# Optimization experiments

Hardware: AMD Instinct MI355X
Metric: run time of the kernel (lower is better)

## Reference

```python
import jax, jax.numpy as jnp
import numpy as np

D_MODEL = 768
D_STATE = 16
D_CONV = 4
EXPAND = 2
D_INNER = EXPAND * D_MODEL  # 1536
DT_RANK = (D_MODEL + 15) // 16  # 48, mamba_ssm default dt_rank='auto'
BATCH = 2
SEQ = 2048


def setup_inputs() -> dict:
    key = jax.random.key(0)
    ks = jax.random.split(key, 9)
    f = lambda k, shp, s=0.02: (jax.random.normal(k, shp, jnp.float32) * s)
    return {
        "x": jax.random.normal(ks[0], (BATCH, SEQ, D_MODEL), jnp.float32),
        "ln_w": jnp.ones((D_MODEL,), jnp.float32),
        "ln_b": jnp.zeros((D_MODEL,), jnp.float32),
        "in_proj_w": f(ks[1], (2 * D_INNER, D_MODEL)),          # no bias (mamba default)
        "conv_w": f(ks[2], (D_INNER, D_CONV), 0.1),              # depthwise causal conv
        "conv_b": f(ks[3], (D_INNER,), 0.1),
        "x_proj_w": f(ks[4], (DT_RANK + 2 * D_STATE, D_INNER)),  # no bias
        "dt_proj_w": f(ks[5], (D_INNER, DT_RANK), 0.1),
        "dt_proj_b": f(ks[6], (D_INNER,), 0.5),
        "A_log": jnp.log(jnp.broadcast_to(
            jnp.arange(1, D_STATE + 1, dtype=jnp.float32), (D_INNER, D_STATE))),  # S4D-real init
        "D": jnp.ones((D_INNER,), jnp.float32),
        "out_proj_w": f(ks[7], (D_MODEL, D_INNER)),              # no bias
    }


def _layernorm(x, w, b, eps=1e-5):
    mu = jnp.mean(x, axis=-1, keepdims=True)
    var = jnp.var(x, axis=-1, keepdims=True)
    return (x - mu) * jax.lax.rsqrt(var + eps) * w + b


def _mamba(xn, in_proj_w, conv_w, conv_b, x_proj_w, dt_proj_w, dt_proj_b,
           A_log, D, out_proj_w):
    B, L, _ = xn.shape
    # input projection -> gate z and ssm branch u
    xz = jnp.einsum("bld,ed->ble", xn, in_proj_w)  # [B,L,2*d_inner]
    u, z = jnp.split(xz, 2, axis=-1)
    # causal depthwise conv1d (kernel D_CONV, left pad D_CONV-1) + SiLU
    up = jnp.pad(u, ((0, 0), (D_CONV - 1, 0), (0, 0)))
    uc = conv_b
    for k in range(D_CONV):  # small fixed tap loop
        uc = uc + conv_w[:, k] * up[:, k:k + L, :]
    uc = jax.nn.silu(uc)  # [B,L,d_inner]
    # data-dependent dt, B, C
    dbl = jnp.einsum("bld,ed->ble", uc, x_proj_w)
    dt, Bm, Cm = jnp.split(dbl, [DT_RANK, DT_RANK + D_STATE], axis=-1)
    delta = jax.nn.softplus(jnp.einsum("blr,dr->bld", dt, dt_proj_w) + dt_proj_b)
    A = -jnp.exp(A_log)  # [d_inner, d_state]

    def step(h, inp):
        u_t, d_t, B_t, C_t = inp  # [B,d_inner],[B,d_inner],[B,d_state],[B,d_state]
        dA = jnp.exp(d_t[..., None] * A)                      # [B,d_inner,d_state]
        h = dA * h + (d_t * u_t)[..., None] * B_t[:, None, :]  # discretized update
        y = jnp.einsum("bds,bs->bd", h, C_t)
        return h, y

    h0 = jnp.zeros((B, D_INNER, D_STATE), xn.dtype)
    xs = (uc.transpose(1, 0, 2), delta.transpose(1, 0, 2),
          Bm.transpose(1, 0, 2), Cm.transpose(1, 0, 2))
    _, ys = jax.lax.scan(step, h0, xs)          # ys: [L,B,d_inner]
    y = ys.transpose(1, 0, 2) + uc * D          # skip connection D*u
    y = y * jax.nn.silu(z)                      # gating
    return jnp.einsum("bld,od->blo", y, out_proj_w)


def reference(x, ln_w, ln_b, in_proj_w, conv_w, conv_b, x_proj_w,
              dt_proj_w, dt_proj_b, A_log, D, out_proj_w):
    xn = _layernorm(x, ln_w, ln_b)
    return x + _mamba(xn, in_proj_w, conv_w, conv_b, x_proj_w,
                      dt_proj_w, dt_proj_b, A_log, D, out_proj_w)
```

## Files before the change

### kernel.cpp

```cpp
#include <hip/hip_runtime.h>
#include <hip/hip_bf16.h>
#include <stdint.h>
#include <math.h>

typedef __hip_bfloat16 bf16;
typedef __attribute__((ext_vector_type(8))) short bf16x8;
typedef __attribute__((ext_vector_type(4))) short s16x4;
typedef __attribute__((ext_vector_type(4))) float f32x4;

#define B_   2
#define L_   2048
#define DM   768
#define DI   1536
#define DS   16
#define M_   (B_ * L_)
#define NC   128
#define LC   (L_ / NC)
#define NSEQ (B_ * DI * DS)
#define KSPLIT 12
#define LOG2E  1.44269504088896f
#define NLOG2E (-1.44269504088896f)

#define GLOAD_LDS16(g, l)                                                     \
  __builtin_amdgcn_global_load_lds(                                           \
      (const __attribute__((address_space(1))) void*)(g),                     \
      (__attribute__((address_space(3))) void*)(l), 16, 0, 0)

__device__ inline float bf2f(short s) {
  union { unsigned int u; float f; } c;
  c.u = ((unsigned int)(unsigned short)s) << 16;
  return c.f;
}

__global__ __launch_bounds__(256) void k_prep(
    const float* __restrict__ x, const float* __restrict__ w,
    const float* __restrict__ b, bf16* __restrict__ xnb,
    const float* __restrict__ ipw, const float* __restrict__ xpw,
    const float* __restrict__ dpw, const float* __restrict__ opw,
    bf16* __restrict__ wib, bf16* __restrict__ wxb,
    bf16* __restrict__ wdb, bf16* __restrict__ wob) {
  const int tid = threadIdx.x;
  if (blockIdx.x < M_) {
    const int m = blockIdx.x;
    const float* row = x + (size_t)m * DM;
    float v0 = row[tid], v1 = row[tid + 256], v2 = row[tid + 512];
    float s1 = v0 + v1 + v2;
    float s2 = v0 * v0 + v1 * v1 + v2 * v2;
    for (int mm = 1; mm < 64; mm <<= 1) {
      s1 += __shfl_xor(s1, mm);
      s2 += __shfl_xor(s2, mm);
    }
    __shared__ float r1s[4], r2s[4];
    int wv = tid >> 6, ln = tid & 63;
    if (ln == 0) { r1s[wv] = s1; r2s[wv] = s2; }
    __syncthreads();
    s1 = r1s[0] + r1s[1] + r1s[2] + r1s[3];
    s2 = r2s[0] + r2s[1] + r2s[2] + r2s[3];
    float mu = s1 * (1.f / 768.f);
    float var = s2 * (1.f / 768.f) - mu * mu;
    float rs = rsqrtf(var + 1e-5f);
    bf16* orow = xnb + (size_t)m * DM;
    orow[tid]       = __float2bfloat16((v0 - mu) * rs * w[tid]       + b[tid]);
    orow[tid + 256] = __float2bfloat16((v1 - mu) * rs * w[tid + 256] + b[tid + 256]);
    orow[tid + 512] = __float2bfloat16((v2 - mu) * rs * w[tid + 512] + b[tid + 512]);
    return;
  }
  const int n1 = 3072 * 768;
  const int n2 = 768 * 1536;
  const int n3 = 128 * 1536;
  const int n4 = 1536 * 64;
  const int total4 = (n1 + n2 + n3 + n4) / 4;
  const int stride = 512 * 256;
  for (int i4 = (blockIdx.x - M_) * 256 + tid; i4 < total4; i4 += stride) {
    int i = i4 * 4;
    f32x4 v = {0.f, 0.f, 0.f, 0.f};
    bf16* dst;
    if (i < n1) {
      v = *(const f32x4*)&ipw[i];
      dst = &wib[i];
    } else if (i < n1 + n2) {
      int j = i - n1;
      v = *(const f32x4*)&opw[j];
      dst = &wob[j];
    } else if (i < n1 + n2 + n3) {
      int j = i - n1 - n2;
      int r = j / 1536, c = j - r * 1536;
      if (r < 80) v = *(const f32x4*)&xpw[r * 1536 + c];
      dst = &wxb[j];
    } else {
      int j = i - n1 - n2 - n3;
      int r = j >> 6, c = j & 63;
      if (c < 48) v = *(const f32x4*)&dpw[r * 48 + c];
      dst = &wdb[j];
    }
    bf16 t[4];
#pragma unroll
    for (int k = 0; k < 4; ++k) t[k] = __float2bfloat16(v[k]);
    *(s16x4*)dst = *(const s16x4*)t;
  }
}

__device__ __forceinline__ void g256_stage_half(
    const bf16* __restrict__ g, int base_row, int K, int k0,
    short* lhalf, int wid, int lane) {
#pragma unroll
  for (int q = 0; q < 2; ++q) {
    int row_l = q * 64 + wid * 8 + (lane >> 3);
    int slot = (lane & 7) ^ (lane >> 3);
    GLOAD_LDS16(g + (size_t)(base_row + row_l) * K + k0 + slot * 8,
                lhalf + q * 4096 + wid * 512);
  }
}

__device__ __forceinline__ bf16x8 g256_ld(const short* bufop, int h, int row_l,
                                          int kk, int lane) {
  int kslot = (kk >> 3) + (lane >> 4);
  int off = h * 8192 + row_l * 64 + ((kslot ^ (lane & 7)) << 3);
  return *(const bf16x8*)&bufop[off];
}

__global__ __launch_bounds__(512) void k_gemm256(
    const bf16* __restrict__ A, const bf16* __restrict__ Bw, int K,
    bf16* __restrict__ C, int ldc) {
  __shared__ short lds[4 * 16384];
  short* A0 = lds;
  short* A1 = lds + 16384;
  short* B0 = lds + 32768;
  short* B1 = lds + 49152;
  const int tid = threadIdx.x, lane = tid & 63, wid = tid >> 6;
  const int wm_i = wid >> 2, wn_i = wid & 3;
  const int m0 = blockIdx.y * 256, n0 = blockIdx.x * 256;
  const int NT = K >> 6;

  f32x4 acc[8][4] = {};

  g256_stage_half(A, m0, K, 0, A0, wid, lane);
  g256_stage_half(A, m0 + 128, K, 0, A0 + 8192, wid, lane);
  g256_stage_half(Bw, n0, K, 0, B0, wid, lane);
  g256_stage_half(Bw, n0 + 128, K, 0, B0 + 8192, wid, lane);
  g256_stage_half(Bw, n0, K, 64, B1, wid, lane);
  g256_stage_half(Bw, n0 + 128, K, 64, B1 + 8192, wid, lane);
  asm volatile("s_waitcnt vmcnt(4)" ::: "memory");
  __builtin_amdgcn_s_barrier();

  for (int t = 0; t < NT; ++t) {
    short* Ab = (t & 1) ? A1 : A0;
    short* Bb = (t & 1) ? B1 : B0;
    short* Anx = (t & 1) ? A0 : A1;

    bf16x8 bfrag[4][2], afr[2][2];
#pragma unroll
    for (int nf = 0; nf < 4; ++nf) {
      int row_l = (wn_i & 1) * 64 + nf * 16 + (lane & 15);
      bfrag[nf][0] = g256_ld(Bb, wn_i >> 1, row_l, 0, lane);
      bfrag[nf][1] = g256_ld(Bb, wn_i >> 1, row_l, 32, lane);
    }
#pragma unroll
    for (int mf = 0; mf < 2; ++mf) {
      int row_l = mf * 16 + (lane & 15);
      afr[mf][0] = g256_ld(Ab, wm_i, row_l, 0, lane);
      afr[mf][1] = g256_ld(Ab, wm_i, row_l, 32, lane);
    }
    if (t + 1 < NT) {
      g256_stage_half(A, m0, K, (t + 1) * 64, Anx, wid, lane);
      g256_stage_half(A, m0 + 128, K, (t + 1) * 64, Anx + 8192, wid, lane);
    }
    __builtin_amdgcn_s_barrier();
    asm volatile("s_waitcnt lgkmcnt(0)" ::: "memory");
    __builtin_amdgcn_sched_barrier(0);
    __builtin_amdgcn_s_setprio(1);
#pragma unroll
    for (int mf = 0; mf < 2; ++mf)
#pragma unroll
      for (int nf = 0; nf < 4; ++nf) {
        acc[mf][nf] = __builtin_amdgcn_mfma_f32_16x16x32_bf16(
            afr[mf][0], bfrag[nf][0], acc[mf][nf], 0, 0, 0);
        acc[mf][nf] = __builtin_amdgcn_mfma_f32_16x16x32_bf16(
            afr[mf][1], bfrag[nf][1], acc[mf][nf], 0, 0, 0);
      }
    __builtin_amdgcn_s_setprio(0);
    __builtin_amdgcn_s_barrier();

#pragma unroll
    for (int p = 1; p < 4; ++p) {
      bf16x8 af2[2][2];
#pragma unroll
      for (int i = 0; i < 2; ++i) {
        int row_l = (p * 2 + i) * 16 + (lane & 15);
        af2[i][0] = g256_ld(Ab, wm_i, row_l, 0, lane);
        af2[i][1] = g256_ld(Ab, wm_i, row_l, 32, lane);
      }
      if (p < 3) {
        if (t + 2 < NT)
          g256_stage_half(Bw, n0 + (p - 1) * 128, K, (t + 2) * 64,
                          Bb + (p - 1) * 8192, wid, lane);
      } else {
        if (t + 2 < NT) {
          asm volatile("s_waitcnt vmcnt(4)" ::: "memory");
        } else {
          asm volatile("s_waitcnt vmcnt(0)" ::: "memory");
        }
      }
      __builtin_amdgcn_s_barrier();
      asm volatile("s_waitcnt lgkmcnt(0)" ::: "memory");
      __builtin_amdgcn_sched_barrier(0);
      __builtin_amdgcn_s_setprio(1);
#pragma unroll
      for (int i = 0; i < 2; ++i) {
        int mf = p * 2 + i;
#pragma unroll
        for (int nf = 0; nf < 4; ++nf) {
          acc[mf][nf] = __builtin_amdgcn_mfma_f32_16x16x32_bf16(
              af2[i][0], bfrag[nf][0], acc[mf][nf], 0, 0, 0);
          acc[mf][nf] = __builtin_amdgcn_mfma_f32_16x16x32_bf16(
              af2[i][1], bfrag[nf][1], acc[mf][nf], 0, 0, 0);
        }
      }
      __builtin_amdgcn_s_setprio(0);
      __builtin_amdgcn_s_barrier();
    }
  }

#pragma unroll
  for (int mf = 0; mf < 8; ++mf) {
    int row = m0 + wm_i * 128 + mf * 16 + ((lane >> 4) << 2);
#pragma unroll
    for (int nf = 0; nf < 4; ++nf) {
      int col = n0 + wn_i * 64 + nf * 16 + (lane & 15);
#pragma unroll
      for (int r = 0; r < 4; ++r)
        C[(size_t)(row + r) * ldc + col] = __float2bfloat16(acc[mf][nf][r]);
    }
  }
}

template <int EPI>
__global__ __launch_bounds__(256) void k_gemm_bt(
    const bf16* __restrict__ A, const bf16* __restrict__ Bw, int M, int N, int K,
    void* __restrict__ Cv, int ldc, const float* __restrict__ aux) {
  __shared__ short As[128 * 64];
  __shared__ short Bs[128 * 64];
  const int tid = threadIdx.x, lane = tid & 63, wv = tid >> 6;

  int bidx = blockIdx.x, bidy = blockIdx.y;
  if (gridDim.z == 1 && (gridDim.y & 7) == 0) {
    const int nx = gridDim.x;
    const int phys = bidy * nx + bidx;
    const int xcd = phys & 7, slot = phys >> 3;
    const int mt_per = gridDim.y >> 3;
    bidy = xcd * mt_per + slot / nx;
    bidx = slot % nx;
  }
  const int m0 = bidy * 128, n0 = bidx * 128;

  const int wm = (wv >> 1) * 64, wn = (wv & 1) * 64;
  const int lrow = lane >> 3, lcol8 = (lane & 7) * 8;
  const int ksl = K / gridDim.z;
  const int koff = ksl * blockIdx.z;

  f32x4 acc[4][4] = {};

  for (int k0 = koff; k0 < koff + ksl; k0 += 64) {
    __syncthreads();
#pragma unroll
    for (int j = 0; j < 4; ++j) {
      int reg = j * 4 + wv;
      int r = reg * 8 + lrow;
      GLOAD_LDS16(A + (size_t)(m0 + r) * K + k0 + lcol8, &As[reg * 8 * 64]);
      GLOAD_LDS16(Bw + (size_t)(n0 + r) * K + k0 + lcol8, &Bs[reg * 8 * 64]);
    }
    asm volatile("s_waitcnt vmcnt(0)" ::: "memory");
    __syncthreads();
#pragma unroll
    for (int kk = 0; kk < 64; kk += 32) {
      bf16x8 af[4], bfr[4];
#pragma unroll
      for (int i = 0; i < 4; ++i)
        af[i] = *(const bf16x8*)&As[(wm + i * 16 + (lane & 15)) * 64 + kk + ((lane >> 4) * 8)];
#pragma unroll
      for (int j = 0; j < 4; ++j)
        bfr[j] = *(const bf16x8*)&Bs[(wn + j * 16 + (lane & 15)) * 64 + kk + ((lane >> 4) * 8)];
#pragma unroll
      for (int i = 0; i < 4; ++i)
#pragma unroll
        for (int j = 0; j < 4; ++j)
          acc[i][j] = __builtin_amdgcn_mfma_f32_16x16x32_bf16(af[i], bfr[j], acc[i][j], 0, 0, 0);
    }
  }

  const size_t zoff = (size_t)blockIdx.z * M * ldc;
#pragma unroll
  for (int i = 0; i < 4; ++i) {
    int row_b = m0 + wm + i * 16 + ((lane >> 4) << 2);
#pragma unroll
    for (int j = 0; j < 4; ++j) {
      int col = n0 + wn + j * 16 + (lane & 15);
#pragma unroll
      for (int r = 0; r < 4; ++r) {
        int row = row_b + r;
        float v = acc[i][j][r];
        if (EPI == 0) {
          ((float*)Cv)[zoff + (size_t)row * ldc + col] = v;
        } else if (EPI == 1) {
          ((bf16*)Cv)[(size_t)row * ldc + col] = __float2bfloat16(v);
        } else if (EPI == 2) {
          float t = v + aux[col];
          float sp = fmaxf(t, 0.f) + __logf(1.f + __expf(-fabsf(t)));
          ((bf16*)Cv)[(size_t)row * ldc + col] = __float2bfloat16(sp);
        } else if (EPI == 3) {
          ((float*)Cv)[(size_t)row * ldc + col] = v + aux[(size_t)row * ldc + col];
        } else {
          ((bf16*)Cv)[zoff + (size_t)row * ldc + col] = __float2bfloat16(v);
        }
      }
    }
  }
}

__global__ __launch_bounds__(256) void k_conv(const bf16* __restrict__ xzb,
                                              const float* __restrict__ cw,
                                              const float* __restrict__ cb,
                                              bf16* __restrict__ ucb) {
  const int idx = blockIdx.x * 256 + threadIdx.x;
  const int mp = idx / (DI / 8);
  const int d8 = (idx - mp * (DI / 8)) * 8;
  const int m0 = mp * 2;
  const int tl = m0 & (L_ - 1);

  float wgt[8][4];
#pragma unroll
  for (int j = 0; j < 8; ++j) {
    f32x4 w4 = *(const f32x4*)&cw[(d8 + j) * 4];
#pragma unroll
    for (int k = 0; k < 4; ++k) wgt[j][k] = w4[k];
  }
  const f32x4* cbv = (const f32x4*)&cb[d8];
  f32x4 cb0 = cbv[0], cb1 = cbv[1];
  float acc0[8], acc1[8];
#pragma unroll
  for (int j = 0; j < 4; ++j) {
    acc0[j] = cb0[j]; acc0[4 + j] = cb1[j];
    acc1[j] = cb0[j]; acc1[4 + j] = cb1[j];
  }

  bf16x8 v[5];
  const bf16x8 z8 = (bf16x8)(short)0;
#pragma unroll
  for (int k = 0; k < 5; ++k) {
    int tt = tl - 3 + k;
    v[k] = (tt >= 0) ? *(const bf16x8*)&xzb[(size_t)(m0 - 3 + k) * 3072 + d8] : z8;
  }
#pragma unroll
  for (int k = 0; k < 4; ++k)
#pragma unroll
    for (int j = 0; j < 8; ++j) {
      acc0[j] += wgt[j][k] * bf2f(v[k][j]);
      acc1[j] += wgt[j][k] * bf2f(v[k + 1][j]);
    }

  bf16 o0[8], o1[8];
#pragma unroll
  for (int j = 0; j < 8; ++j) {
    o0[j] = __float2bfloat16(acc0[j] / (1.f + __expf(-acc0[j])));
    o1[j] = __float2bfloat16(acc1[j] / (1.f + __expf(-acc1[j])));
  }
  *(bf16x8*)&ucb[(size_t)m0 * DI + d8]       = *(bf16x8*)o0;
  *(bf16x8*)&ucb[(size_t)(m0 + 1) * DI + d8] = *(bf16x8*)o1;
}

__global__ __launch_bounds__(256) void k_xred(const float* __restrict__ xpart,
                                              float* __restrict__ dbl,
                                              bf16* __restrict__ dtb) {
  const int idx = blockIdx.x * 256 + threadIdx.x;
  const int m = idx >> 7, c = idx & 127;
  float sum = 0.f;
#pragma unroll
  for (int s = 0; s < KSPLIT; ++s) sum += xpart[(size_t)s * (M_ * 128) + idx];
  dbl[idx] = sum;
  if (c < 64) dtb[m * 64 + c] = __float2bfloat16(c < 48 ? sum : 0.f);
}

__global__ __launch_bounds__(256) void k_ored(const bf16* __restrict__ op,
                                              const float* __restrict__ x,
                                              float* __restrict__ out) {
  const int i8 = (blockIdx.x * 256 + threadIdx.x) * 8;
  bf16x8 p0 = *(const bf16x8*)&op[i8];
  bf16x8 p1 = *(const bf16x8*)&op[(size_t)M_ * DM + i8];
  const f32x4* xp = (const f32x4*)&x[i8];
  f32x4 x0 = xp[0], x1 = xp[1];
  f32x4 o0, o1;
#pragma unroll
  for (int j = 0; j < 4; ++j) {
    o0[j] = x0[j] + bf2f(p0[j])     + bf2f(p1[j]);
    o1[j] = x1[j] + bf2f(p0[4 + j]) + bf2f(p1[4 + j]);
  }
  f32x4* outp = (f32x4*)&out[i8];
  outp[0] = o0;
  outp[1] = o1;
}

#define DA_CHAIN(dtval)                                                       \
  float r1 = __builtin_amdgcn_exp2f((dtval) * NLOG2E);                        \
  float r2 = r1 * r1, r3 = r2 * r1, r4 = r2 * r2;                             \
  float r5 = r4 * r1, r6 = r4 * r2, r7 = r4 * r3, r8 = r4 * r4;               \
  float dA[16] = {r1, r2, r3, r4, r5, r6, r7, r8,                             \
                  r8 * r1, r8 * r2, r8 * r3, r8 * r4,                         \
                  r8 * r5, r8 * r6, r8 * r7, r8 * r8};

__global__ __launch_bounds__(256) void k_scan1(
    const bf16* __restrict__ dlt, const bf16* __restrict__ ucb,
    const float* __restrict__ dbl,
    bf16* __restrict__ Qb, float* __restrict__ dts) {
  const int blk = blockIdx.x;
  const int cg = blk % (DI / 256);
  const int ch = (blk / (DI / 256)) % NC;
  const int b  = blk / ((DI / 256) * NC);
  const int d  = cg * 256 + threadIdx.x;
  const int t0 = ch * LC;
  __shared__ float sB[LC][16];
  {
    int t = threadIdx.x >> 4, j = threadIdx.x & 15;
    sB[t][j] = dbl[(size_t)(b * L_ + t0 + t) * 128 + 48 + j];
  }
  const bf16* dp = dlt + (size_t)(b * L_ + t0) * DI + d;
  const bf16* up = ucb + (size_t)(b * L_ + t0) * DI + d;
  float dtv[LC], uv[LC];
#pragma unroll
  for (int t = 0; t < LC; ++t) {
    dtv[t] = __bfloat162float(dp[(size_t)t * DI]);
    uv[t]  = __bfloat162float(up[(size_t)t * DI]);
  }
  float h[16];
#pragma unroll
  for (int s = 0; s < 16; ++s) h[s] = 0.f;
  __syncthreads();
  float dtsum = 0.f;
#pragma unroll
  for (int t = 0; t < LC; ++t) {
    float du = dtv[t] * uv[t];
    dtsum += dtv[t];
    const f32x4* bp = (const f32x4*)&sB[t][0];
    f32x4 Bv[4] = {bp[0], bp[1], bp[2], bp[3]};
    DA_CHAIN(dtv[t]);
#pragma unroll
    for (int s = 0; s < 16; ++s)
      h[s] = dA[s] * h[s] + du * Bv[s >> 2][s & 3];
  }
  size_t base = (size_t)ch * NSEQ + (size_t)(b * DI + d) * DS;
  bf16 qs[16];
#pragma unroll
  for (int s = 0; s < 16; ++s) qs[s] = __float2bfloat16(h[s]);
  *(bf16x8*)&Qb[base]     = *(bf16x8*)&qs[0];
  *(bf16x8*)&Qb[base + 8] = *(bf16x8*)&qs[8];
  dts[(size_t)ch * (B_ * DI) + b * DI + d] = dtsum;
}

__global__ __launch_bounds__(256) void k_scan2(const bf16* __restrict__ Qb,
                                               bf16* __restrict__ Hb,
                                               const float* __restrict__ dts,
                                               const float* __restrict__ A_log) {
  const int gid = blockIdx.x * 256 + threadIdx.x;
  const int bd0 = (blockIdx.x * 256) >> 4;
  __shared__ float sDts[NC][16];
  for (int i = threadIdx.x; i < NC * 16; i += 256) {
    int c = i >> 4, k = i & 15;
    sDts[c][k] = dts[(size_t)c * (B_ * DI) + bd0 + k];
  }
  const float a2 = -__expf(A_log[gid % (DI * DS)]) * LOG2E;
  const int bdl = threadIdx.x >> 4;
  __syncthreads();
  float h = 0.f;
  for (int c0 = 0; c0 < NC; c0 += 8) {
    float q[8];
#pragma unroll
    for (int k = 0; k < 8; ++k)
      q[k] = __bfloat162float(Qb[(size_t)(c0 + k) * NSEQ + gid]);
#pragma unroll
    for (int k = 0; k < 8; ++k) {
      float P = __builtin_amdgcn_exp2f(a2 * sDts[c0 + k][bdl]);
      Hb[(size_t)(c0 + k) * NSEQ + gid] = __float2bfloat16(h);
      h = P * h + q[k];
    }
  }
}

__global__ __launch_bounds__(256) void k_scan3(
    const bf16* __restrict__ dlt, const bf16* __restrict__ ucb,
    const bf16* __restrict__ xzb, const float* __restrict__ dbl,
    const float* __restrict__ Dp,
    const bf16* __restrict__ Hb, bf16* __restrict__ ybf) {
  const int blk = blockIdx.x;
  const int cg = blk % (DI / 256);
  const int ch = (blk / (DI / 256)) % NC;
  const int b  = blk / ((DI / 256) * NC);
  const int d  = cg * 256 + threadIdx.x;
  const int t0 = ch * LC;
  __shared__ float sBC[LC][32];
  for (int i = threadIdx.x; i < LC * 32; i += 256) {
    int t = i >> 5, j = i & 31;
    sBC[t][j] = dbl[(size_t)(b * L_ + t0 + t) * 128 + 48 + j];
  }
  const bf16* dp = dlt + (size_t)(b * L_ + t0) * DI + d;
  const bf16* up = ucb + (size_t)(b * L_ + t0) * DI + d;
  const bf16* zp = xzb + (size_t)(b * L_ + t0) * 3072 + DI + d;
  float dtv[LC], uv[LC], zv[LC];
#pragma unroll
  for (int t = 0; t < LC; ++t) {
    dtv[t] = __bfloat162float(dp[(size_t)t * DI]);
    uv[t]  = __bfloat162float(up[(size_t)t * DI]);
    zv[t]  = __bfloat162float(zp[(size_t)t * 3072]);
  }
  float h[16];
  const bf16* Hp = Hb + (size_t)ch * NSEQ + (size_t)(b * DI + d) * DS;
  bf16x8 h0 = *(const bf16x8*)&Hp[0];
  bf16x8 h1 = *(const bf16x8*)&Hp[8];
#pragma unroll
  for (int s = 0; s < 16; ++s) h[s] = bf2f(s < 8 ? h0[s] : h1[s - 8]);
  const float Dd = Dp[d];
  __syncthreads();
  bf16* yp = ybf + (size_t)(b * L_ + t0) * DI + d;
#pragma unroll
  for (int t = 0; t < LC; ++t) {
    float du = dtv[t] * uv[t];
    const f32x4* bc = (const f32x4*)&sBC[t][0];
    f32x4 Bv[4]  = {bc[0], bc[1], bc[2], bc[3]};
    f32x4 Cv4[4] = {bc[4], bc[5], bc[6], bc[7]};
    DA_CHAIN(dtv[t]);
    float y = 0.f;
#pragma unroll
    for (int s = 0; s < 16; ++s) {
      h[s] = dA[s] * h[s] + du * Bv[s >> 2][s & 3];
      y += h[s] * Cv4[s >> 2][s & 3];
    }
    y += Dd * uv[t];
    float g = zv[t] / (1.f + __expf(-zv[t]));
    yp[(size_t)t * DI] = __float2bfloat16(y * g);
  }
}

extern "C" void kernel_launch(void* const* d_in, const int* in_sizes, int n_in,
                              void* d_out, int out_size, void* d_ws, size_t ws_size,
                              hipStream_t stream) {
  const float* x    = (const float*)d_in[0];
  const float* lnw  = (const float*)d_in[1];
  const float* lnb  = (const float*)d_in[2];
  const float* ipw  = (const float*)d_in[3];
  const float* cw   = (const float*)d_in[4];
  const float* cb   = (const float*)d_in[5];
  const float* xpw  = (const float*)d_in[6];
  const float* dpw  = (const float*)d_in[7];
  const float* dpb  = (const float*)d_in[8];
  const float* alog = (const float*)d_in[9];
  const float* Dp   = (const float*)d_in[10];
  const float* opw  = (const float*)d_in[11];

  char* p = (char*)d_ws;
  auto alloc = [&](size_t bytes) {
    char* r = p;
    p += (bytes + 255) & ~(size_t)255;
    return r;
  };
  bf16* xnb  = (bf16*)alloc((size_t)M_ * DM * 2);
  bf16* wib  = (bf16*)alloc((size_t)3072 * 768 * 2);
  bf16* wxb  = (bf16*)alloc((size_t)128 * 1536 * 2);
  bf16* wdb  = (bf16*)alloc((size_t)1536 * 64 * 2);
  bf16* wob  = (bf16*)alloc((size_t)768 * 1536 * 2);
  bf16* xzb  = (bf16*)alloc((size_t)M_ * 3072 * 2);
  bf16* ucb  = (bf16*)alloc((size_t)M_ * DI * 2);
  float* dbl = (float*)alloc((size_t)M_ * 128 * 4);
  bf16* dtb  = (bf16*)alloc((size_t)M_ * 64 * 2);
  bf16* dlt  = (bf16*)alloc((size_t)M_ * DI * 2);
  bf16* ybf  = (bf16*)alloc((size_t)M_ * DI * 2);
  bf16* Qb   = (bf16*)alloc((size_t)NC * NSEQ * 2);
  bf16* Hb   = (bf16*)alloc((size_t)NC * NSEQ * 2);
  float* dts = (float*)alloc((size_t)NC * B_ * DI * 4);
  float* xpart = (float*)Qb;
  bf16* opart = Qb;

  k_prep<<<M_ + 512, 256, 0, stream>>>(x, lnw, lnb, xnb, ipw, xpw, dpw, opw,
                                       wib, wxb, wdb, wob);

  dim3 g1(3072 / 256, M_ / 256);
  k_gemm256<<<g1, 512, 0, stream>>>(xnb, wib, 768, xzb, 3072);

  k_conv<<<(M_ / 2) * (DI / 8) / 256, 256, 0, stream>>>(xzb, cw, cb, ucb);

  dim3 g2(1, M_ / 128, KSPLIT);
  k_gemm_bt<0><<<g2, 256, 0, stream>>>(ucb, wxb, M_, 128, 1536, xpart, 128, nullptr);

  k_xred<<<(M_ * 128) / 256, 256, 0, stream>>>(xpart, dbl, dtb);

  dim3 g3(1536 / 128, M_ / 128);
  k_gemm_bt<2><<<g3, 256, 0, stream>>>(dtb, wdb, M_, 1536, 64, dlt, 1536, dpb);

  const int nblk = B_ * NC * (DI / 256);
  k_scan1<<<nblk, 256, 0, stream>>>(dlt, ucb, dbl, Qb, dts);
  k_scan2<<<NSEQ / 256, 256, 0, stream>>>(Qb, Hb, dts, alog);
  k_scan3<<<nblk, 256, 0, stream>>>(dlt, ucb, xzb, dbl, Dp, Hb, ybf);

  dim3 g4(768 / 128, M_ / 128, 2);
  k_gemm_bt<4><<<g4, 256, 0, stream>>>(ybf, wob, M_, 768, 1536, opart, 768, nullptr);

  k_ored<<<(M_ * DM / 8) / 256, 256, 0, stream>>>(opart, x, (float*)d_out);
}
```

Baseline: 152.0 us.

## Restructure 256 GEMM main loop, swizzle block order, store x_proj partials in bf16

The 256x256 in_proj GEMM main loop drops from four sub-phases with barriers to two larger phases per K-tile, each doing 32 MFMAs. B-tile prefetches move into the two phases. A blockIdx remap spreads consecutive workgroups across XCD-sized groups to improve L2 locality. The split-K x_proj GEMM now writes bf16 partials (EPI 4) instead of fp32, which halves partial traffic at the cost of precision in the reduced dt/B/C values. The larger fragment arrays raise register pressure.

```diff
diff --git a/kernel.cpp b/kernel.cpp
--- a/kernel.cpp
+++ b/kernel.cpp
@@ -123,32 +123,44 @@
     const bf16* __restrict__ A, const bf16* __restrict__ Bw, int K,
     bf16* __restrict__ C, int ldc) {
   __shared__ short lds[4 * 16384];
-  short* A0 = lds;
-  short* A1 = lds + 16384;
-  short* B0 = lds + 32768;
-  short* B1 = lds + 49152;
+  short* Abuf0 = lds;
+  short* Abuf1 = lds + 16384;
+  short* Bbuf0 = lds + 32768;
+  short* Bbuf1 = lds + 49152;
   const int tid = threadIdx.x, lane = tid & 63, wid = tid >> 6;
   const int wm_i = wid >> 2, wn_i = wid & 3;
-  const int m0 = blockIdx.y * 256, n0 = blockIdx.x * 256;
+
+  int bidx = blockIdx.x, bidy = blockIdx.y;
+  {
+    int nx = gridDim.x;
+    int nwg = nx * gridDim.y;
+    if ((nwg & 7) == 0) {
+      int phys = bidy * nx + bidx;
+      int lin = (phys & 7) * (nwg >> 3) + (phys >> 3);
+      bidy = lin / nx;
+      bidx = lin - bidy * nx;
+    }
+  }
+  const int m0 = bidy * 256, n0 = bidx * 256;
   const int NT = K >> 6;
 
   f32x4 acc[8][4] = {};
 
-  g256_stage_half(A, m0, K, 0, A0, wid, lane);
-  g256_stage_half(A, m0 + 128, K, 0, A0 + 8192, wid, lane);
-  g256_stage_half(Bw, n0, K, 0, B0, wid, lane);
-  g256_stage_half(Bw, n0 + 128, K, 0, B0 + 8192, wid, lane);
-  g256_stage_half(Bw, n0, K, 64, B1, wid, lane);
-  g256_stage_half(Bw, n0 + 128, K, 64, B1 + 8192, wid, lane);
+  g256_stage_half(A, m0, K, 0, Abuf0, wid, lane);
+  g256_stage_half(A, m0 + 128, K, 0, Abuf0 + 8192, wid, lane);
+  g256_stage_half(Bw, n0, K, 0, Bbuf0, wid, lane);
+  g256_stage_half(Bw, n0 + 128, K, 0, Bbuf0 + 8192, wid, lane);
+  g256_stage_half(Bw, n0, K, 64, Bbuf1, wid, lane);
+  g256_stage_half(Bw, n0 + 128, K, 64, Bbuf1 + 8192, wid, lane);
   asm volatile("s_waitcnt vmcnt(4)" ::: "memory");
   __builtin_amdgcn_s_barrier();
 
   for (int t = 0; t < NT; ++t) {
-    short* Ab = (t & 1) ? A1 : A0;
-    short* Bb = (t & 1) ? B1 : B0;
-    short* Anx = (t & 1) ? A0 : A1;
-
-    bf16x8 bfrag[4][2], afr[2][2];
+    short* Ab  = (t & 1) ? Abuf1 : Abuf0;
+    short* Bb  = (t & 1) ? Bbuf1 : Bbuf0;
+    short* Anx = (t & 1) ? Abuf0 : Abuf1;
+
+    bf16x8 bfrag[4][2], afA[4][2];
 #pragma unroll
     for (int nf = 0; nf < 4; ++nf) {
       int row_l = (wn_i & 1) * 64 + nf * 16 + (lane & 15);
@@ -156,69 +168,57 @@
       bfrag[nf][1] = g256_ld(Bb, wn_i >> 1, row_l, 32, lane);
     }
 #pragma unroll
-    for (int mf = 0; mf < 2; ++mf) {
+    for (int mf = 0; mf < 4; ++mf) {
       int row_l = mf * 16 + (lane & 15);
-      afr[mf][0] = g256_ld(Ab, wm_i, row_l, 0, lane);
-      afr[mf][1] = g256_ld(Ab, wm_i, row_l, 32, lane);
+      afA[mf][0] = g256_ld(Ab, wm_i, row_l, 0, lane);
+      afA[mf][1] = g256_ld(Ab, wm_i, row_l, 32, lane);
     }
     if (t + 1 < NT) {
       g256_stage_half(A, m0, K, (t + 1) * 64, Anx, wid, lane);
       g256_stage_half(A, m0 + 128, K, (t + 1) * 64, Anx + 8192, wid, lane);
     }
+    asm volatile("s_waitcnt lgkmcnt(0)" ::: "memory");
     __builtin_amdgcn_s_barrier();
-    asm volatile("s_waitcnt lgkmcnt(0)" ::: "memory");
-    __builtin_amdgcn_sched_barrier(0);
+    if (t + 2 < NT)
+      g256_stage_half(Bw, n0, K, (t + 2) * 64, Bb, wid, lane);
     __builtin_amdgcn_s_setprio(1);
 #pragma unroll
-    for (int mf = 0; mf < 2; ++mf)
+    for (int mf = 0; mf < 4; ++mf)
 #pragma unroll
       for (int nf = 0; nf < 4; ++nf) {
         acc[mf][nf] = __builtin_amdgcn_mfma_f32_16x16x32_bf16(
-            afr[mf][0], bfrag[nf][0], acc[mf][nf], 0, 0, 0);
+            afA[mf][0], bfrag[nf][0], acc[mf][nf], 0, 0, 0);
         acc[mf][nf] = __builtin_amdgcn_mfma_f32_16x16x32_bf16(
-            afr[mf][1], bfrag[nf][1], acc[mf][nf], 0, 0, 0);
+            afA[mf][1], bfrag[nf][1], acc[mf][nf], 0, 0, 0);
       }
     __builtin_amdgcn_s_setprio(0);
+
+    bf16x8 afB[4][2];
+#pragma unroll
+    for (int mf = 0; mf < 4; ++mf) {
+      int row_l = (mf + 4) * 16 + (lane & 15);
+      afB[mf][0] = g256_ld(Ab, wm_i, row_l, 0, lane);
+      afB[mf][1] = g256_ld(Ab, wm_i, row_l, 32, lane);
+    }
+    if (t + 2 < NT)
+      g256_stage_half(Bw, n0 + 128, K, (t + 2) * 64, Bb + 8192, wid, lane);
+    __builtin_amdgcn_s_setprio(1);
+#pragma unroll
+    for (int mf = 0; mf < 4; ++mf)
+#pragma unroll
+      for (int nf = 0; nf < 4; ++nf) {
+        acc[mf + 4][nf] = __builtin_amdgcn_mfma_f32_16x16x32_bf16(
+            afB[mf][0], bfrag[nf][0], acc[mf + 4][nf], 0, 0, 0);
+        acc[mf + 4][nf] = __builtin_amdgcn_mfma_f32_16x16x32_bf16(
+            afB[mf][1], bfrag[nf][1], acc[mf + 4][nf], 0, 0, 0);
+      }
+    __builtin_amdgcn_s_setprio(0);
+    if (t + 2 < NT) {
+      asm volatile("s_waitcnt vmcnt(4)" ::: "memory");
+    } else {
+      asm volatile("s_waitcnt vmcnt(0)" ::: "memory");
+    }
     __builtin_amdgcn_s_barrier();
-
-#pragma unroll
-    for (int p = 1; p < 4; ++p) {
-      bf16x8 af2[2][2];
-#pragma unroll
-      for (int i = 0; i < 2; ++i) {
-        int row_l = (p * 2 + i) * 16 + (lane & 15);
-        af2[i][0] = g256_ld(Ab, wm_i, row_l, 0, lane);
-        af2[i][1] = g256_ld(Ab, wm_i, row_l, 32, lane);
-      }
-      if (p < 3) {
-        if (t + 2 < NT)
-          g256_stage_half(Bw, n0 + (p - 1) * 128, K, (t + 2) * 64,
-                          Bb + (p - 1) * 8192, wid, lane);
-      } else {
-        if (t + 2 < NT) {
-          asm volatile("s_waitcnt vmcnt(4)" ::: "memory");
-        } else {
-          asm volatile("s_waitcnt vmcnt(0)" ::: "memory");
-        }
-      }
-      __builtin_amdgcn_s_barrier();
-      asm volatile("s_waitcnt lgkmcnt(0)" ::: "memory");
-      __builtin_amdgcn_sched_barrier(0);
-      __builtin_amdgcn_s_setprio(1);
-#pragma unroll
-      for (int i = 0; i < 2; ++i) {
-        int mf = p * 2 + i;
-#pragma unroll
-        for (int nf = 0; nf < 4; ++nf) {
-          acc[mf][nf] = __builtin_amdgcn_mfma_f32_16x16x32_bf16(
-              af2[i][0], bfrag[nf][0], acc[mf][nf], 0, 0, 0);
-          acc[mf][nf] = __builtin_amdgcn_mfma_f32_16x16x32_bf16(
-              af2[i][1], bfrag[nf][1], acc[mf][nf], 0, 0, 0);
-        }
-      }
-      __builtin_amdgcn_s_setprio(0);
-      __builtin_amdgcn_s_barrier();
-    }
   }
 
 #pragma unroll
@@ -368,14 +368,15 @@
   *(bf16x8*)&ucb[(size_t)(m0 + 1) * DI + d8] = *(bf16x8*)o1;
 }
 
-__global__ __launch_bounds__(256) void k_xred(const float* __restrict__ xpart,
+__global__ __launch_bounds__(256) void k_xred(const bf16* __restrict__ xpart,
                                               float* __restrict__ dbl,
                                               bf16* __restrict__ dtb) {
   const int idx = blockIdx.x * 256 + threadIdx.x;
   const int m = idx >> 7, c = idx & 127;
   float sum = 0.f;
 #pragma unroll
-  for (int s = 0; s < KSPLIT; ++s) sum += xpart[(size_t)s * (M_ * 128) + idx];
+  for (int s = 0; s < KSPLIT; ++s)
+    sum += __bfloat162float(xpart[(size_t)s * (M_ * 128) + idx]);
   dbl[idx] = sum;
   if (c < 64) dtb[m * 64 + c] = __float2bfloat16(c < 48 ? sum : 0.f);
 }
@@ -574,7 +575,7 @@
   bf16* Qb   = (bf16*)alloc((size_t)NC * NSEQ * 2);
   bf16* Hb   = (bf16*)alloc((size_t)NC * NSEQ * 2);
   float* dts = (float*)alloc((size_t)NC * B_ * DI * 4);
-  float* xpart = (float*)Qb;
+  bf16* xpart = Qb;
   bf16* opart = Qb;
 
   k_prep<<<M_ + 512, 256, 0, stream>>>(x, lnw, lnb, xnb, ipw, xpw, dpw, opw,
@@ -586,7 +587,7 @@
   k_conv<<<(M_ / 2) * (DI / 8) / 256, 256, 0, stream>>>(xzb, cw, cb, ucb);
 
   dim3 g2(1, M_ / 128, KSPLIT);
-  k_gemm_bt<0><<<g2, 256, 0, stream>>>(ucb, wxb, M_, 128, 1536, xpart, 128, nullptr);
+  k_gemm_bt<4><<<g2, 256, 0, stream>>>(ucb, wxb, M_, 128, 1536, xpart, 128, nullptr);
 
   k_xred<<<(M_ * 128) / 256, 256, 0, stream>>>(xpart, dbl, dtb);
 
```

Result: faster. 148.6 us (median of 2 runs) (-2.2%).
